# Kernel tuning notes

Measured on AMD Instinct MI355X. Metric: run time of the kernel, lower is better.

Reference implementation:

```python
import jax, jax.numpy as jnp
import numpy as np

N_Q = 8  # number of residual quantization levels


def setup_inputs() -> dict:
    key = jax.random.key(0)
    k1, k2 = jax.random.split(key)
    hidden_states = jax.random.normal(k1, (8192, 128), dtype=jnp.float32)
    codebooks = jax.random.normal(k2, (N_Q, 256, 128), dtype=jnp.float32)
    return {"hidden_states": hidden_states, "codebooks": codebooks}


def reference(hidden_states, codebooks):
    """Residual VQ encode: per level, nearest codebook entry by L2, subtract, accumulate.

    hidden_states: [N, D]; codebooks: [n_q, bins, D].
    Returns (codes [n_q, N] int, quantized [N, D]).
    """
    residual = hidden_states
    quantized = jnp.zeros_like(hidden_states)
    codes = []
    for i in range(N_Q):  # small fixed loop over structurally distinct levels
        codebook = codebooks[i]  # [bins, D]
        # squared L2 distance, same math as the original broadcasted form
        dist = jnp.sum((residual[:, None, :] - codebook[None, :, :]) ** 2, axis=-1)  # [N, bins]
        idx = jnp.argmin(dist, axis=-1)  # [N]
        chosen = codebook[idx]  # [N, D]
        quantized = quantized + chosen
        residual = residual - chosen
        codes.append(idx)
    return jnp.stack(codes, axis=0), quantized
```

## Files before the change

kernel.cpp:

```cpp
#include <hip/hip_runtime.h>

#define NQ 8
#define BINS 256
#define D 128
#define RPB 32
#define THREADS 512
#define RSTRIDE 132
#define FREG 520

typedef short s8v __attribute__((ext_vector_type(8)));
typedef float f4v __attribute__((ext_vector_type(4)));

static __device__ __forceinline__ unsigned short bf16_rtne(float x) {
    unsigned u = __float_as_uint(x);
    unsigned r = (u + 0x7fffu + ((u >> 16) & 1u)) >> 16;
    return (unsigned short)r;
}
static __device__ __forceinline__ float bf16_to_f(unsigned short h) {
    return __uint_as_float(((unsigned)h) << 16);
}
struct Split3 { short h, m, l; };
static __device__ __forceinline__ Split3 split3(float x) {
    Split3 s;
    unsigned short hb = bf16_rtne(x);
    float r1 = x - bf16_to_f(hb);
    unsigned short mb = bf16_rtne(r1);
    unsigned short lb = bf16_rtne(r1 - bf16_to_f(mb));
    s.h = (short)hb; s.m = (short)mb; s.l = (short)lb;
    return s;
}
static __device__ __forceinline__ unsigned long long shfl_xor_u64(unsigned long long v, int mask) {
    int lo = (int)(unsigned)(v & 0xffffffffull);
    int hi = (int)(unsigned)(v >> 32);
    lo = __shfl_xor(lo, mask, 64);
    hi = __shfl_xor(hi, mask, 64);
    return ((unsigned long long)(unsigned)hi << 32) | (unsigned)lo;
}
static __device__ __forceinline__ unsigned long long u64min(unsigned long long a, unsigned long long b) {
    return a < b ? a : b;
}

__global__ __launch_bounds__(256) void rvq_prep(
    const float* __restrict__ cb, short* __restrict__ cb_hi,
    short* __restrict__ cb_mid, short* __restrict__ cb_lo,
    float* __restrict__ c2)
{
    __shared__ float st[16 * RSTRIDE];
    const int L = blockIdx.x >> 4;
    const int o = blockIdx.x & 15;
    const int t = threadIdx.x;

    const float4* src = (const float4*)(cb + ((size_t)L * BINS + o * 16) * D);
    #pragma unroll
    for (int i = 0; i < 2; ++i) {
        int f4 = i * 256 + t;
        int row = f4 >> 5, c4 = f4 & 31;
        float4 v = src[f4];
        float* d = &st[row * RSTRIDE + c4 * 4];
        d[0] = v.x; d[1] = v.y; d[2] = v.z; d[3] = v.w;
    }
    __syncthreads();

    const int bin = t >> 4;
    const int kc  = t & 15;
    const float* p = &st[bin * RSTRIDE + kc * 8];
    s8v h8, m8, l8;
    float s = 0.f;
    #pragma unroll
    for (int j = 0; j < 8; ++j) {
        float x = p[j];
        Split3 sp = split3(x);
        h8[j] = sp.h; m8[j] = sp.m; l8[j] = sp.l;
        s = fmaf(x, x, s);
    }
    int idx = (L * 16 + kc) * BINS + (o * 16 + bin);
    ((s8v*)cb_hi)[idx]  = h8;
    ((s8v*)cb_mid)[idx] = m8;
    ((s8v*)cb_lo)[idx]  = l8;
    s += __shfl_xor(s, 1, 64);
    s += __shfl_xor(s, 2, 64);
    s += __shfl_xor(s, 4, 64);
    s += __shfl_xor(s, 8, 64);
    if (kc == 0) c2[L * BINS + o * 16 + bin] = s;
}

static __device__ __forceinline__ void frag_store(
    const float* rres, short* ah, short* am, short* al, int rr_, int g8)
{
    s8v h8, m8, l8;
    #pragma unroll
    for (int j = 0; j < 8; ++j) {
        Split3 sp = split3(rres[j]);
        h8[j] = sp.h; m8[j] = sp.m; l8[j] = sp.l;
    }
    int q = g8 & 3;
    int reg = (rr_ >> 4) * 4 + (g8 >> 2);
    int idx16 = q * 16 + (((rr_ & 15) + 4 * q) & 15);
    int off = reg * FREG + idx16 * 8;
    *(s8v*)&ah[off] = h8;
    *(s8v*)&am[off] = m8;
    *(s8v*)&al[off] = l8;
}

__global__ __launch_bounds__(THREADS, 2) void rvq_kernel(
    const float* __restrict__ hidden,
    const float* __restrict__ cb_f32,
    const short* __restrict__ cb_hi,
    const short* __restrict__ cb_mid,
    const short* __restrict__ cb_lo,
    const float* __restrict__ c2p,
    float* __restrict__ out_codes,
    float* __restrict__ out_quant,
    int N)
{
    __shared__ short ah[8 * FREG];
    __shared__ short am[8 * FREG];
    __shared__ short al[8 * FREG];
    __shared__ unsigned long long redw[RPB][8];

    const int t = threadIdx.x;
    const int w = t >> 6;
    const int l = t & 63;
    const int quad = l >> 4;
    const int m = l & 15;
    const int row0 = blockIdx.x * RPB;
    const int woff = w * 32;
    const int rr_ = t >> 4;
    const int g8 = t & 15;

    float rres[8];
    {
        const float4* hp = (const float4*)(hidden + (size_t)(row0 + rr_) * D + g8 * 8);
        float4 v0 = hp[0], v1 = hp[1];
        rres[0] = v0.x; rres[1] = v0.y; rres[2] = v0.z; rres[3] = v0.w;
        rres[4] = v1.x; rres[5] = v1.y; rres[6] = v1.z; rres[7] = v1.w;
    }
    frag_store(rres, ah, am, al, rr_, g8);

    const s8v* bhp = (const s8v*)cb_hi;
    const s8v* bmp = (const s8v*)cb_mid;
    const s8v* blp = (const s8v*)cb_lo;

    for (int level = 0; level < NQ; ++level) {
        s8v bh[2][4], bm[2][4], bl[2][4];
        float c2v[2];
        #pragma unroll
        for (int nt = 0; nt < 2; ++nt) {
            int bin = woff + nt * 16 + m;
            c2v[nt] = c2p[level * BINS + bin];
            #pragma unroll
            for (int ks = 0; ks < 4; ++ks) {
                int idx = (level * 16 + ks * 4 + quad) * BINS + bin;
                bh[nt][ks] = bhp[idx];
                bm[nt][ks] = bmp[idx];
                bl[nt][ks] = blp[idx];
            }
        }
        __syncthreads();

        s8v afh[2][4], afm[2][4], afl[2][4];
        #pragma unroll
        for (int mt = 0; mt < 2; ++mt)
            #pragma unroll
            for (int ks = 0; ks < 4; ++ks) {
                int idx16 = quad * 16 + ((m + 4 * quad) & 15);
                int off = (mt * 4 + ks) * FREG + idx16 * 8;
                afh[mt][ks] = *(const s8v*)&ah[off];
                afm[mt][ks] = *(const s8v*)&am[off];
                afl[mt][ks] = *(const s8v*)&al[off];
            }

        unsigned long long best[2][4];
        #pragma unroll
        for (int mt = 0; mt < 2; ++mt)
            #pragma unroll
            for (int i = 0; i < 4; ++i) best[mt][i] = ~0ull;

        #pragma unroll
        for (int nt = 0; nt < 2; ++nt) {
            const int bin = woff + nt * 16 + m;
            #pragma unroll
            for (int mt = 0; mt < 2; ++mt) {
                f4v a0 = {0.f, 0.f, 0.f, 0.f};
                f4v a1 = {0.f, 0.f, 0.f, 0.f};
                f4v a2 = {0.f, 0.f, 0.f, 0.f};
                #pragma unroll
                for (int ks = 0; ks < 4; ++ks) {
                    a0 = __builtin_amdgcn_mfma_f32_16x16x32_bf16(afh[mt][ks], bh[nt][ks], a0, 0, 0, 0);
                    a1 = __builtin_amdgcn_mfma_f32_16x16x32_bf16(afh[mt][ks], bm[nt][ks], a1, 0, 0, 0);
                    a1 = __builtin_amdgcn_mfma_f32_16x16x32_bf16(afm[mt][ks], bh[nt][ks], a1, 0, 0, 0);
                    a2 = __builtin_amdgcn_mfma_f32_16x16x32_bf16(afm[mt][ks], bm[nt][ks], a2, 0, 0, 0);
                    a2 = __builtin_amdgcn_mfma_f32_16x16x32_bf16(afh[mt][ks], bl[nt][ks], a2, 0, 0, 0);
                    a2 = __builtin_amdgcn_mfma_f32_16x16x32_bf16(afl[mt][ks], bh[nt][ks], a2, 0, 0, 0);
                }
                #pragma unroll
                for (int i = 0; i < 4; ++i) {
                    float dot = a0[i] + (a1[i] + a2[i]);
                    float k = fmaf(-2.f, dot, c2v[nt]);
                    unsigned u = __float_as_uint(k);
                    u = (u & 0x80000000u) ? ~u : (u | 0x80000000u);
                    unsigned long long key = ((unsigned long long)u << 32) | (unsigned)bin;
                    best[mt][i] = u64min(best[mt][i], key);
                }
            }
        }

        #pragma unroll
        for (int mt = 0; mt < 2; ++mt)
            #pragma unroll
            for (int i = 0; i < 4; ++i) {
                unsigned long long p = best[mt][i];
                p = u64min(p, shfl_xor_u64(p, 1));
                p = u64min(p, shfl_xor_u64(p, 2));
                p = u64min(p, shfl_xor_u64(p, 4));
                p = u64min(p, shfl_xor_u64(p, 8));
                if (m == 0) redw[mt * 16 + quad * 4 + i][w] = p;
            }
        __syncthreads();

        unsigned long long mn = redw[rr_][0];
        #pragma unroll
        for (int j = 1; j < 8; ++j) mn = u64min(mn, redw[rr_][j]);
        const int wb = (int)(mn & 0xffffffffull);
        if (g8 == 0)
            out_codes[(size_t)level * N + row0 + rr_] = (float)wb;

        {
            const float4* cp = (const float4*)(cb_f32 + ((size_t)level * BINS + wb) * D + g8 * 8);
            float4 c0 = cp[0], c1 = cp[1];
            rres[0] -= c0.x; rres[1] -= c0.y; rres[2] -= c0.z; rres[3] -= c0.w;
            rres[4] -= c1.x; rres[5] -= c1.y; rres[6] -= c1.z; rres[7] -= c1.w;
        }
        frag_store(rres, ah, am, al, rr_, g8);
    }

    {
        const float4* hp = (const float4*)(hidden + (size_t)(row0 + rr_) * D + g8 * 8);
        float4 v0 = hp[0], v1 = hp[1];
        float4 q0, q1;
        q0.x = v0.x - rres[0]; q0.y = v0.y - rres[1]; q0.z = v0.z - rres[2]; q0.w = v0.w - rres[3];
        q1.x = v1.x - rres[4]; q1.y = v1.y - rres[5]; q1.z = v1.z - rres[6]; q1.w = v1.w - rres[7];
        float4* op = (float4*)(out_quant + (size_t)(row0 + rr_) * D + g8 * 8);
        op[0] = q0; op[1] = q1;
    }
}

extern "C" void kernel_launch(void* const* d_in, const int* in_sizes, int n_in,
                              void* d_out, int out_size, void* d_ws, size_t ws_size,
                              hipStream_t stream) {
    const float* hidden    = (const float*)d_in[0];
    const float* codebooks = (const float*)d_in[1];
    float* out = (float*)d_out;
    const int N = in_sizes[0] / D;
    float* out_codes = out;
    float* out_quant = out + (size_t)NQ * N;

    char* ws = (char*)d_ws;
    short* cb_hi  = (short*)ws;
    short* cb_mid = (short*)(ws +  512 * 1024);
    short* cb_lo  = (short*)(ws + 1024 * 1024);
    float* c2     = (float*)(ws + 1536 * 1024);

    rvq_prep<<<dim3(NQ * 16), 256, 0, stream>>>(codebooks, cb_hi, cb_mid, cb_lo, c2);
    rvq_kernel<<<dim3(N / RPB), THREADS, 0, stream>>>(
        hidden, codebooks, cb_hi, cb_mid, cb_lo, c2, out_codes, out_quant, N);
}
```

Before: 110.5 us.

## Double warps per block, prefetch next-level codebook, use DPP argmin reduction

```diff
diff --git a/kernel.cpp b/kernel.cpp
--- a/kernel.cpp
+++ b/kernel.cpp
@@ -4,11 +4,12 @@
 #define BINS 256
 #define D 128
 #define RPB 32
-#define THREADS 512
+#define THREADS 1024
 #define RSTRIDE 132
 #define FREG 520
 
 typedef short s8v __attribute__((ext_vector_type(8)));
+typedef short s4v __attribute__((ext_vector_type(4)));
 typedef float f4v __attribute__((ext_vector_type(4)));
 
 static __device__ __forceinline__ unsigned short bf16_rtne(float x) {
@@ -29,15 +30,16 @@
     s.h = (short)hb; s.m = (short)mb; s.l = (short)lb;
     return s;
 }
-static __device__ __forceinline__ unsigned long long shfl_xor_u64(unsigned long long v, int mask) {
-    int lo = (int)(unsigned)(v & 0xffffffffull);
-    int hi = (int)(unsigned)(v >> 32);
-    lo = __shfl_xor(lo, mask, 64);
-    hi = __shfl_xor(hi, mask, 64);
-    return ((unsigned long long)(unsigned)hi << 32) | (unsigned)lo;
-}
 static __device__ __forceinline__ unsigned long long u64min(unsigned long long a, unsigned long long b) {
     return a < b ? a : b;
+}
+static __device__ __forceinline__ unsigned dpp_row_min16(unsigned v) {
+    unsigned t;
+    t = (unsigned)__builtin_amdgcn_update_dpp(0, (int)v, 0xB1,  0xF, 0xF, true); v = v < t ? v : t;
+    t = (unsigned)__builtin_amdgcn_update_dpp(0, (int)v, 0x4E,  0xF, 0xF, true); v = v < t ? v : t;
+    t = (unsigned)__builtin_amdgcn_update_dpp(0, (int)v, 0x124, 0xF, 0xF, true); v = v < t ? v : t;
+    t = (unsigned)__builtin_amdgcn_update_dpp(0, (int)v, 0x128, 0xF, 0xF, true); v = v < t ? v : t;
+    return v;
 }
 
 __global__ __launch_bounds__(256) void rvq_prep(
@@ -84,25 +86,41 @@
     if (kc == 0) c2[L * BINS + o * 16 + bin] = s;
 }
 
-static __device__ __forceinline__ void frag_store(
-    const float* rres, short* ah, short* am, short* al, int rr_, int g8)
-{
-    s8v h8, m8, l8;
-    #pragma unroll
-    for (int j = 0; j < 8; ++j) {
+static __device__ __forceinline__ void frag_store4(
+    const float* rres, short* ah, short* am, short* al, int rr_, int g8, int half)
+{
+    s4v h4, m4, l4;
+    #pragma unroll
+    for (int j = 0; j < 4; ++j) {
         Split3 sp = split3(rres[j]);
-        h8[j] = sp.h; m8[j] = sp.m; l8[j] = sp.l;
+        h4[j] = sp.h; m4[j] = sp.m; l4[j] = sp.l;
     }
     int q = g8 & 3;
     int reg = (rr_ >> 4) * 4 + (g8 >> 2);
     int idx16 = q * 16 + (((rr_ & 15) + 4 * q) & 15);
-    int off = reg * FREG + idx16 * 8;
-    *(s8v*)&ah[off] = h8;
-    *(s8v*)&am[off] = m8;
-    *(s8v*)&al[off] = l8;
-}
-
-__global__ __launch_bounds__(THREADS, 2) void rvq_kernel(
+    int off = reg * FREG + idx16 * 8 + half * 4;
+    *(s4v*)&ah[off] = h4;
+    *(s4v*)&am[off] = m4;
+    *(s4v*)&al[off] = l4;
+}
+
+static __device__ __forceinline__ void issue_b(
+    int lv, int bin, int quad,
+    const s8v* __restrict__ bhp, const s8v* __restrict__ bmp, const s8v* __restrict__ blp,
+    const float* __restrict__ c2p,
+    s8v bh[4], s8v bm[4], s8v bl[4], float& c2v)
+{
+    c2v = c2p[lv * BINS + bin];
+    #pragma unroll
+    for (int ks = 0; ks < 4; ++ks) {
+        int idx = (lv * 16 + ks * 4 + quad) * BINS + bin;
+        bh[ks] = bhp[idx];
+        bm[ks] = bmp[idx];
+        bl[ks] = blp[idx];
+    }
+}
+
+__global__ __launch_bounds__(THREADS) void rvq_kernel(
     const float* __restrict__ hidden,
     const float* __restrict__ cb_f32,
     const short* __restrict__ cb_hi,
@@ -116,7 +134,7 @@
     __shared__ short ah[8 * FREG];
     __shared__ short am[8 * FREG];
     __shared__ short al[8 * FREG];
-    __shared__ unsigned long long redw[RPB][8];
+    __shared__ __align__(16) unsigned long long redw[RPB][18];
 
     const int t = threadIdx.x;
     const int w = t >> 6;
@@ -124,124 +142,114 @@
     const int quad = l >> 4;
     const int m = l & 15;
     const int row0 = blockIdx.x * RPB;
-    const int woff = w * 32;
-    const int rr_ = t >> 4;
-    const int g8 = t & 15;
-
-    float rres[8];
+    const int woff = w * 16;
+    const int bin = woff + m;
+    const int rr_ = t >> 5;
+    const int gd  = t & 31;
+    const int g8  = gd >> 1;
+    const int half = gd & 1;
+
+    float rres[4];
     {
-        const float4* hp = (const float4*)(hidden + (size_t)(row0 + rr_) * D + g8 * 8);
-        float4 v0 = hp[0], v1 = hp[1];
-        rres[0] = v0.x; rres[1] = v0.y; rres[2] = v0.z; rres[3] = v0.w;
-        rres[4] = v1.x; rres[5] = v1.y; rres[6] = v1.z; rres[7] = v1.w;
-    }
-    frag_store(rres, ah, am, al, rr_, g8);
+        const float4* hp = (const float4*)(hidden + (size_t)(row0 + rr_) * D + gd * 4);
+        float4 v = *hp;
+        rres[0] = v.x; rres[1] = v.y; rres[2] = v.z; rres[3] = v.w;
+    }
+    frag_store4(rres, ah, am, al, rr_, g8, half);
 
     const s8v* bhp = (const s8v*)cb_hi;
     const s8v* bmp = (const s8v*)cb_mid;
     const s8v* blp = (const s8v*)cb_lo;
 
+    s8v bh[4], bm[4], bl[4];
+    float c2v;
+    issue_b(0, bin, quad, bhp, bmp, blp, c2p, bh, bm, bl, c2v);
+
     for (int level = 0; level < NQ; ++level) {
-        s8v bh[2][4], bm[2][4], bl[2][4];
-        float c2v[2];
+        __syncthreads();
+
+        unsigned ucand[2][4];
+        const int idx16 = quad * 16 + ((m + 4 * quad) & 15);
         #pragma unroll
-        for (int nt = 0; nt < 2; ++nt) {
-            int bin = woff + nt * 16 + m;
-            c2v[nt] = c2p[level * BINS + bin];
+        for (int mt = 0; mt < 2; ++mt) {
+            s8v afh[4], afm[4], afl[4];
             #pragma unroll
             for (int ks = 0; ks < 4; ++ks) {
-                int idx = (level * 16 + ks * 4 + quad) * BINS + bin;
-                bh[nt][ks] = bhp[idx];
-                bm[nt][ks] = bmp[idx];
-                bl[nt][ks] = blp[idx];
+                int off = (mt * 4 + ks) * FREG + idx16 * 8;
+                afh[ks] = *(const s8v*)&ah[off];
+                afm[ks] = *(const s8v*)&am[off];
+                afl[ks] = *(const s8v*)&al[off];
+            }
+            f4v a0 = {0.f, 0.f, 0.f, 0.f};
+            f4v a1 = {0.f, 0.f, 0.f, 0.f};
+            f4v a2 = {0.f, 0.f, 0.f, 0.f};
+            #pragma unroll
+            for (int ks = 0; ks < 4; ++ks) {
+                a0 = __builtin_amdgcn_mfma_f32_16x16x32_bf16(afh[ks], bh[ks], a0, 0, 0, 0);
+                a1 = __builtin_amdgcn_mfma_f32_16x16x32_bf16(afh[ks], bm[ks], a1, 0, 0, 0);
+                a1 = __builtin_amdgcn_mfma_f32_16x16x32_bf16(afm[ks], bh[ks], a1, 0, 0, 0);
+                a2 = __builtin_amdgcn_mfma_f32_16x16x32_bf16(afm[ks], bm[ks], a2, 0, 0, 0);
+                a2 = __builtin_amdgcn_mfma_f32_16x16x32_bf16(afh[ks], bl[ks], a2, 0, 0, 0);
+                a2 = __builtin_amdgcn_mfma_f32_16x16x32_bf16(afl[ks], bh[ks], a2, 0, 0, 0);
+            }
+            #pragma unroll
+            for (int i = 0; i < 4; ++i) {
+                float dot = a0[i] + (a1[i] + a2[i]);
+                float k = fmaf(-2.f, dot, c2v);
+                unsigned u = __float_as_uint(k);
+                u = (u & 0x80000000u) ? ~u : (u | 0x80000000u);
+                ucand[mt][i] = u;
             }
         }
-        __syncthreads();
-
-        s8v afh[2][4], afm[2][4], afl[2][4];
+
         #pragma unroll
         for (int mt = 0; mt < 2; ++mt)
             #pragma unroll
-            for (int ks = 0; ks < 4; ++ks) {
-                int idx16 = quad * 16 + ((m + 4 * quad) & 15);
-                int off = (mt * 4 + ks) * FREG + idx16 * 8;
-                afh[mt][ks] = *(const s8v*)&ah[off];
-                afm[mt][ks] = *(const s8v*)&am[off];
-                afl[mt][ks] = *(const s8v*)&al[off];
-            }
-
-        unsigned long long best[2][4];
-        #pragma unroll
-        for (int mt = 0; mt < 2; ++mt)
-            #pragma unroll
-            for (int i = 0; i < 4; ++i) best[mt][i] = ~0ull;
-
-        #pragma unroll
-        for (int nt = 0; nt < 2; ++nt) {
-            const int bin = woff + nt * 16 + m;
-            #pragma unroll
-            for (int mt = 0; mt < 2; ++mt) {
-                f4v a0 = {0.f, 0.f, 0.f, 0.f};
-                f4v a1 = {0.f, 0.f, 0.f, 0.f};
-                f4v a2 = {0.f, 0.f, 0.f, 0.f};
-                #pragma unroll
-                for (int ks = 0; ks < 4; ++ks) {
-                    a0 = __builtin_amdgcn_mfma_f32_16x16x32_bf16(afh[mt][ks], bh[nt][ks], a0, 0, 0, 0);
-                    a1 = __builtin_amdgcn_mfma_f32_16x16x32_bf16(afh[mt][ks], bm[nt][ks], a1, 0, 0, 0);
-                    a1 = __builtin_amdgcn_mfma_f32_16x16x32_bf16(afm[mt][ks], bh[nt][ks], a1, 0, 0, 0);
-                    a2 = __builtin_amdgcn_mfma_f32_16x16x32_bf16(afm[mt][ks], bm[nt][ks], a2, 0, 0, 0);
-                    a2 = __builtin_amdgcn_mfma_f32_16x16x32_bf16(afh[mt][ks], bl[nt][ks], a2, 0, 0, 0);
-                    a2 = __builtin_amdgcn_mfma_f32_16x16x32_bf16(afl[mt][ks], bh[nt][ks], a2, 0, 0, 0);
-                }
-                #pragma unroll
-                for (int i = 0; i < 4; ++i) {
-                    float dot = a0[i] + (a1[i] + a2[i]);
-                    float k = fmaf(-2.f, dot, c2v[nt]);
-                    unsigned u = __float_as_uint(k);
-                    u = (u & 0x80000000u) ? ~u : (u | 0x80000000u);
-                    unsigned long long key = ((unsigned long long)u << 32) | (unsigned)bin;
-                    best[mt][i] = u64min(best[mt][i], key);
-                }
-            }
+            for (int i = 0; i < 4; ++i) {
+                unsigned v = ucand[mt][i];
+                unsigned r = dpp_row_min16(v);
+                unsigned long long mk = __ballot(v == r);
+                unsigned grp = (unsigned)(mk >> (quad * 16)) & 0xffffu;
+                int bmin = woff + __builtin_ctz(grp);
+                if (m == 0)
+                    redw[mt * 16 + quad * 4 + i][w] =
+                        ((unsigned long long)r << 32) | (unsigned)bmin;
+            }
+        __syncthreads();
+
+        if (level + 1 < NQ)
+            issue_b(level + 1, bin, quad, bhp, bmp, blp, c2p, bh, bm, bl, c2v);
+
+        unsigned long long mn;
+        {
+            const ulonglong2* rp = (const ulonglong2*)&redw[rr_][0];
+            ulonglong2 p0 = rp[0], p1 = rp[1], p2 = rp[2], p3 = rp[3];
+            ulonglong2 p4 = rp[4], p5 = rp[5], p6 = rp[6], p7 = rp[7];
+            unsigned long long a = u64min(u64min(u64min(p0.x, p0.y), u64min(p1.x, p1.y)),
+                                          u64min(u64min(p2.x, p2.y), u64min(p3.x, p3.y)));
+            unsigned long long b = u64min(u64min(u64min(p4.x, p4.y), u64min(p5.x, p5.y)),
+                                          u64min(u64min(p6.x, p6.y), u64min(p7.x, p7.y)));
+            mn = u64min(a, b);
         }
-
-        #pragma unroll
-        for (int mt = 0; mt < 2; ++mt)
-            #pragma unroll
-            for (int i = 0; i < 4; ++i) {
-                unsigned long long p = best[mt][i];
-                p = u64min(p, shfl_xor_u64(p, 1));
-                p = u64min(p, shfl_xor_u64(p, 2));
-                p = u64min(p, shfl_xor_u64(p, 4));
-                p = u64min(p, shfl_xor_u64(p, 8));
-                if (m == 0) redw[mt * 16 + quad * 4 + i][w] = p;
-            }
-        __syncthreads();
-
-        unsigned long long mn = redw[rr_][0];
-        #pragma unroll
-        for (int j = 1; j < 8; ++j) mn = u64min(mn, redw[rr_][j]);
         const int wb = (int)(mn & 0xffffffffull);
-        if (g8 == 0)
+        if (gd == 0)
             out_codes[(size_t)level * N + row0 + rr_] = (float)wb;
 
         {
-            const float4* cp = (const float4*)(cb_f32 + ((size_t)level * BINS + wb) * D + g8 * 8);
-            float4 c0 = cp[0], c1 = cp[1];
-            rres[0] -= c0.x; rres[1] -= c0.y; rres[2] -= c0.z; rres[3] -= c0.w;
-            rres[4] -= c1.x; rres[5] -= c1.y; rres[6] -= c1.z; rres[7] -= c1.w;
+            const float4* cp = (const float4*)(cb_f32 + ((size_t)level * BINS + wb) * D + gd * 4);
+            float4 c = *cp;
+            rres[0] -= c.x; rres[1] -= c.y; rres[2] -= c.z; rres[3] -= c.w;
         }
-        frag_store(rres, ah, am, al, rr_, g8);
+        if (level + 1 < NQ)
+            frag_store4(rres, ah, am, al, rr_, g8, half);
     }
 
     {
-        const float4* hp = (const float4*)(hidden + (size_t)(row0 + rr_) * D + g8 * 8);
-        float4 v0 = hp[0], v1 = hp[1];
-        float4 q0, q1;
-        q0.x = v0.x - rres[0]; q0.y = v0.y - rres[1]; q0.z = v0.z - rres[2]; q0.w = v0.w - rres[3];
-        q1.x = v1.x - rres[4]; q1.y = v1.y - rres[5]; q1.z = v1.z - rres[6]; q1.w = v1.w - rres[7];
-        float4* op = (float4*)(out_quant + (size_t)(row0 + rr_) * D + g8 * 8);
-        op[0] = q0; op[1] = q1;
+        const float4* hp = (const float4*)(hidden + (size_t)(row0 + rr_) * D + gd * 4);
+        float4 v = *hp;
+        float4 q;
+        q.x = v.x - rres[0]; q.y = v.y - rres[1]; q.z = v.z - rres[2]; q.w = v.w - rres[3];
+        *(float4*)(out_quant + (size_t)(row0 + rr_) * D + gd * 4) = q;
     }
 }
 
```

Measured after the change: 106.7 us. 1.04x faster.
